# Kernel tuning notes

Measured on AMD Instinct MI355X. Metric: run time of the kernel, lower is better.

Reference implementation:

```python
import jax, jax.numpy as jnp
import numpy as np
from jax import lax

N, C_IN, DIMS, NW, T, H, W = 8, 64, 64, 8, 16, 64, 64
BN_EPS = 1e-5


def setup_inputs() -> dict:
    key = jax.random.key(0)
    ks = jax.random.split(key, 10)
    # kaiming-ish scales
    w_scale = (2.0 / (C_IN * 27)) ** 0.5
    return {
        "x": jax.random.normal(ks[0], (N, C_IN, T, H, W), dtype=jnp.float32),
        "weights": jax.random.normal(ks[1], (NW, DIMS, C_IN, 3, 3, 3), dtype=jnp.float32) * w_scale,
        "biases": jax.random.normal(ks[2], (NW, DIMS), dtype=jnp.float32),
        "se_w1": jax.random.normal(ks[3], (16, C_IN, 5, 5), dtype=jnp.float32) * (2.0 / (C_IN * 25)) ** 0.5,
        "se_b1": jnp.zeros((16,), dtype=jnp.float32),
        "se_w2": jax.random.normal(ks[4], (32, 16, 5, 5), dtype=jnp.float32) * (2.0 / (16 * 25)) ** 0.5,
        "se_b2": jnp.zeros((32,), dtype=jnp.float32),
        "lin_w": jax.random.normal(ks[5], (NW, 32), dtype=jnp.float32) * (1.0 / 32) ** 0.5,
        "lin_b": jnp.zeros((NW,), dtype=jnp.float32),
        "bn_gamma": jnp.ones((DIMS,), dtype=jnp.float32),
        "bn_beta": jnp.zeros((DIMS,), dtype=jnp.float32),
        "epochs_num": 15,
    }


def _forward(x, weights, biases, se_w1, se_b1, se_w2, se_b2, lin_w, lin_b, bn_gamma, bn_beta, epochs_num):
    tau = 30.0 - 2.9 * epochs_num if epochs_num < 10 else 1.0
    # std over temporal axis (torch.std -> unbiased, ddof=1): [n, c, h, w]
    std_x = jnp.std(x, axis=2, ddof=1)
    # squeeze-expand attention branch
    dn2d = ("NCHW", "OIHW", "NCHW")
    h1 = lax.conv_general_dilated(std_x, se_w1, (1, 1), "VALID", dimension_numbers=dn2d)
    h1 = jax.nn.relu(h1 + se_b1[None, :, None, None])
    h2 = lax.conv_general_dilated(h1, se_w2, (1, 1), "VALID", dimension_numbers=dn2d)
    h2 = jax.nn.relu(h2 + se_b2[None, :, None, None])
    pooled = jnp.max(h2, axis=(2, 3))                      # [n, 32]
    logits = pooled @ lin_w.T + lin_b                       # [n, num_weights]
    phi = jax.nn.softmax(logits / tau, axis=1)
    # per-sample dynamic kernels / biases
    dyn_w = jnp.einsum("bn,ncidhw->bcidhw", phi, weights)   # [n, dims, c_in, 3,3,3]
    dyn_b = phi @ biases                                    # [n, dims]
    # grouped conv3d (groups = n) == per-sample conv3d via vmap
    dn3d = ("NCDHW", "OIDHW", "NCDHW")
    def one_conv(xi, wi):
        return lax.conv_general_dilated(xi[None], wi, (1, 1, 1), "SAME", dimension_numbers=dn3d)[0]
    y = jax.vmap(one_conv)(x, dyn_w)                        # [n, dims, t, h, w]
    y = y + dyn_b[:, :, None, None, None]
    # BatchNorm3d (training mode, batch stats, biased var)
    mean = jnp.mean(y, axis=(0, 2, 3, 4))
    var = jnp.var(y, axis=(0, 2, 3, 4))
    b = lambda v: v[None, :, None, None, None]
    y = (y - b(mean)) * b(bn_gamma) * lax.rsqrt(b(var) + BN_EPS) + b(bn_beta)
    return jax.nn.relu(y)


def reference(x, weights, biases, se_w1, se_b1, se_w2, se_b2, lin_w, lin_b, bn_gamma, bn_beta, epochs_num):
    return _forward(x, weights, biases, se_w1, se_b1, se_w2, se_b2, lin_w, lin_b, bn_gamma, bn_beta, epochs_num)
```

## Files before the change

### kernel.cpp

```cpp
#include <hip/hip_runtime.h>
#include <hip/hip_bf16.h>
#include <math.h>

#define N_   8
#define CIN_ 64
#define DIMS_ 64
#define NW_  8
#define T_   16
#define H_   64
#define W_   64
#define HW_  (H_ * W_)
#define THW_ (T_ * HW_)

typedef short bf16x8 __attribute__((ext_vector_type(8)));
typedef float f32x16 __attribute__((ext_vector_type(16)));
typedef int   i32x4v __attribute__((ext_vector_type(4)));
typedef float f32x4v __attribute__((ext_vector_type(4)));

__device__ __forceinline__ unsigned short f2bf(float f) {
    union { float f; unsigned u; } a; a.f = f;
    unsigned r = a.u + 0x7fffu + ((a.u >> 16) & 1u);
    return (unsigned short)(r >> 16);
}
__device__ __forceinline__ float bf2f(unsigned short u) {
    union { unsigned u; float f; } a; a.u = ((unsigned)u) << 16; return a.f;
}

#define CS8_ 8
#define HS8_ (66 * CS8_)
#define TS8_ (10 * HS8_)
#define XSH_ (3 * TS8_)
#define WLH_ (28 * 64 * 8)

__host__ __device__ constexpr int OXc(int tap) {
    int tt = tap > 26 ? 26 : tap;
    return (tt / 9) * TS8_ + ((tt % 9) / 3) * HS8_ + ((tt % 3) - 1) * CS8_;
}

__global__ __launch_bounds__(128) void stdxb_f4(
    const float* __restrict__ x, float* __restrict__ std_x,
    unsigned short* __restrict__ xb, float* __restrict__ sums,
    unsigned* __restrict__ pooled,
    const float* __restrict__ w1, const float* __restrict__ w2,
    float* __restrict__ w1t, float* __restrict__ w2t)
{
    __shared__ unsigned short xsl[16 * 64 * 8];
    const int h = blockIdx.x, c8 = blockIdx.y, n = blockIdx.z;
    const int tid = threadIdx.x;
    const int bf = blockIdx.x + (blockIdx.y << 6) + ((int)blockIdx.z << 9);
    if (bf == 0) {
        sums[tid] = 0.f;
        pooled[tid] = 0u;
        pooled[tid + 128] = 0u;
    }
    if (bf < 300) {
        int i = bf * 128 + tid;
        if (i < 25600) {
            int k = i / 1600, c = (i / 25) % 64, tap = i % 25;
            w1t[(c * 25 + tap) * 16 + k] = w1[i];
        } else if (i < 38400) {
            int j = i - 25600;
            int o = j / 400, c = (j / 25) % 16, tap = j % 25;
            w2t[(c * 25 + tap) * 32 + o] = w2[j];
        }
    }
    const int c = tid >> 4, w4 = tid & 15;
    const int cin = c8 * 8 + c;
    const float* px = x + (((size_t)(n * 64 + cin)) << 16) + (h << 6) + (w4 << 2);
    float s[4] = {0.f, 0.f, 0.f, 0.f}, s2[4] = {0.f, 0.f, 0.f, 0.f};
#pragma unroll
    for (int t = 0; t < T_; ++t) {
        float4 v = *(const float4*)(px + t * HW_);
        float vv[4] = {v.x, v.y, v.z, v.w};
#pragma unroll
        for (int j = 0; j < 4; ++j) {
            s[j] += vv[j];
            s2[j] += vv[j] * vv[j];
            xsl[(t << 9) + (((j << 4) | w4) << 3) + c] = f2bf(vv[j]);
        }
    }
    float4 sd;
#pragma unroll
    for (int j = 0; j < 4; ++j) {
        float var = (s2[j] - s[j] * s[j] * (1.0f / 16.0f)) * (1.0f / 15.0f);
        (&sd.x)[j] = sqrtf(fmaxf(var, 0.f));
    }
    *(float4*)(std_x + (((size_t)(n * 64 + cin)) << 12) + (h << 6) + (w4 << 2)) = sd;
    __syncthreads();
    const int4* src = (const int4*)xsl;
    int4* dst = (int4*)(xb + ((size_t)((n * 8 + c8) * 16) << 12) * 8);
#pragma unroll
    for (int k = 0; k < 8; ++k) {
        int j2 = tid + (k << 7);
        int t = j2 >> 6, q = j2 & 63;
        int ww = ((q & 15) << 2) | (q >> 4);
        dst[((t << 6) + h) * 64 + ww] = src[j2];
    }
}

__global__ __launch_bounds__(256) void se_conv1c(const float* __restrict__ std_x,
        const float* __restrict__ w1t, const float* __restrict__ b1, float* __restrict__ h1) {
    __shared__ float red[3][64][8];
    const int n = blockIdx.y, ks = blockIdx.z * 8;
    const int iq = threadIdx.x & 63, cq = threadIdx.x >> 6;
    const int ij = blockIdx.x * 64 + iq;
    float acc[8];
#pragma unroll
    for (int q = 0; q < 8; ++q) acc[q] = 0.f;
    if (ij < 3600) {
        int i = ij / 60, j = ij - i * 60;
        const float* xn = std_x + (size_t)n * CIN_ * HW_ + i * W_ + j;
        for (int c = cq * 16; c < cq * 16 + 16; ++c) {
            const float* xc = xn + c * HW_;
            float xv[25];
#pragma unroll
            for (int u = 0; u < 5; ++u)
#pragma unroll
                for (int v = 0; v < 5; ++v) xv[u * 5 + v] = xc[u * W_ + v];
            const float* wc = w1t + c * 400 + ks;
#pragma unroll
            for (int tap = 0; tap < 25; ++tap)
#pragma unroll
                for (int q = 0; q < 8; ++q)
                    acc[q] = fmaf(xv[tap], wc[tap * 16 + q], acc[q]);
        }
    }
    if (cq > 0) {
#pragma unroll
        for (int q = 0; q < 8; ++q) red[cq - 1][iq][q] = acc[q];
    }
    __syncthreads();
    if (cq == 0 && ij < 3600) {
#pragma unroll
        for (int q = 0; q < 8; ++q) {
            float a = acc[q] + red[0][iq][q] + red[1][iq][q] + red[2][iq][q] + b1[ks + q];
            h1[((size_t)(n * 16 + ks + q)) * 3600 + ij] = fmaxf(a, 0.f);
        }
    }
}

__global__ __launch_bounds__(256) void se_conv2c(const float* __restrict__ h1,
        const float* __restrict__ w2t, const float* __restrict__ b2,
        unsigned* __restrict__ pooled) {
    __shared__ float red[3][64][8];
    const int n = blockIdx.y, os = blockIdx.z * 8;
    const int iq = threadIdx.x & 63, cq = threadIdx.x >> 6;
    const int ij = blockIdx.x * 64 + iq;
    const int i = ij / 56, j = ij - i * 56;
    float acc[8];
#pragma unroll
    for (int q = 0; q < 8; ++q) acc[q] = 0.f;
    const float* xn = h1 + (size_t)n * 16 * 3600 + i * 60 + j;
    for (int c = cq * 4; c < cq * 4 + 4; ++c) {
        const float* xc = xn + c * 3600;
        float xv[25];
#pragma unroll
        for (int u = 0; u < 5; ++u)
#pragma unroll
            for (int v = 0; v < 5; ++v) xv[u * 5 + v] = xc[u * 60 + v];
        const float* wc = w2t + c * 800 + os;
#pragma unroll
        for (int tap = 0; tap < 25; ++tap)
#pragma unroll
            for (int q = 0; q < 8; ++q)
                acc[q] = fmaf(xv[tap], wc[tap * 32 + q], acc[q]);
    }
    if (cq > 0) {
#pragma unroll
        for (int q = 0; q < 8; ++q) red[cq - 1][iq][q] = acc[q];
    }
    __syncthreads();
    if (cq == 0) {
#pragma unroll
        for (int q = 0; q < 8; ++q) {
            float a = fmaxf(acc[q] + red[0][iq][q] + red[1][iq][q] + red[2][iq][q] + b2[os + q], 0.f);
#pragma unroll
            for (int m = 1; m < 64; m <<= 1) a = fmaxf(a, __shfl_xor(a, m, 64));
            if (iq == 0) atomicMax(&pooled[n * 32 + os + q], __float_as_uint(a));
        }
    }
}

__global__ __launch_bounds__(256) void dyn_w_head(
    const float* __restrict__ weights, const float* __restrict__ pooled,
    const float* __restrict__ lin_w, const float* __restrict__ lin_b,
    const float* __restrict__ biases, const int* __restrict__ epochs,
    unsigned short* __restrict__ wtb2, float* __restrict__ dyn_b) {
    __shared__ float slog[8][8];
    __shared__ float sphi[64];
    const int tid = threadIdx.x;
    const int e = epochs[0];
    const float tau = (e < 10) ? (30.0f - 2.9f * (float)e) : 1.0f;
    if (tid < 64) {
        int b = tid >> 3, m = tid & 7;
        float acc = lin_b[m];
#pragma unroll
        for (int k = 0; k < 32; ++k) acc += pooled[b * 32 + k] * lin_w[m * 32 + k];
        slog[b][m] = acc / tau;
    }
    __syncthreads();
    if (tid < 8) {
        float mx = slog[tid][0];
#pragma unroll
        for (int m = 1; m < 8; ++m) mx = fmaxf(mx, slog[tid][m]);
        float ex[8], ssum = 0.f;
#pragma unroll
        for (int m = 0; m < 8; ++m) { ex[m] = expf(slog[tid][m] - mx); ssum += ex[m]; }
        float inv = 1.0f / ssum;
#pragma unroll
        for (int m = 0; m < 8; ++m) sphi[tid * 8 + m] = ex[m] * inv;
    }
    __syncthreads();
    if (blockIdx.x < 64) {
        int b = blockIdx.x >> 3, c8 = blockIdx.x & 7;
        unsigned* dst = (unsigned*)(wtb2 + (size_t)b * 114688 + (size_t)(c8 * 28 + 27) * 512);
        dst[tid] = 0u;
    }
    if (blockIdx.x == 0) {
#pragma unroll
        for (int idx = tid; idx < 512; idx += 256) {
            int b = idx >> 6, d = idx & 63;
            float a = 0.f;
#pragma unroll
            for (int m = 0; m < 8; ++m) a += sphi[b * 8 + m] * biases[m * DIMS_ + d];
            dyn_b[idx] = a;
        }
    }
    int f = blockIdx.x * 256 + tid;
    if (f >= 110592) return;
    int tap = f % 27, cin = (f / 27) & 63, co = f / 1728;
    float wv[8];
#pragma unroll
    for (int m = 0; m < 8; ++m) wv[m] = weights[(size_t)m * 110592 + f];
    size_t dbase = (size_t)(cin >> 3) * 14336 + tap * 512 + co * 8 + (cin & 7);
#pragma unroll
    for (int b = 0; b < 8; ++b) {
        float acc = 0.f;
#pragma unroll
        for (int m = 0; m < 8; ++m) acc += sphi[b * 8 + m] * wv[m];
        wtb2[(size_t)b * 114688 + dbase] = f2bf(acc);
    }
}

__global__ __launch_bounds__(256, 2) void conv3d_mfma5(
    const unsigned short* __restrict__ xb,
    const unsigned short* __restrict__ wtb2,
    const float* __restrict__ dynb,
    float* __restrict__ y,
    unsigned short* __restrict__ ybf,
    float* __restrict__ sums)
{
    __shared__ __align__(16) unsigned short xs[XSH_];
    __shared__ __align__(16) unsigned short wl[WLH_];
    __shared__ float bnred[128];

    const int flat = blockIdx.x;
    const int n = flat & 7;
    const int hb = (flat >> 3) & 7;
    const int t = flat >> 6;
    const int stag = (((flat >> 3) ^ (flat >> 8)) & 1) * 4;
    const int tid = threadIdx.x;
    const int lane = tid & 63, wid = tid >> 6;
    const int lane31 = lane & 31, tau = lane >> 5;
    const int hbase = hb * 8;

    for (int i = tid; i < XSH_ / 8; i += 256)
        *(int4*)&xs[i * 8] = (int4){0, 0, 0, 0};
    if (tid < 128) bnred[tid] = 0.f;

    const unsigned short* xnb = xb + (size_t)n * 4194304;
    const unsigned short* wnb = wtb2 + (size_t)n * 114688;

    f32x16 acc[2][4];
#pragma unroll
    for (int ci = 0; ci < 2; ++ci)
#pragma unroll
        for (int s = 0; s < 4; ++s)
            acc[ci][s] = (f32x16)(0.f);

    const int aBase = tau * 512 + lane31 * 8;
    int bsp[4];
#pragma unroll
    for (int s = 0; s < 4; ++s)
        bsp[s] = (2 * wid + (s >> 1)) * HS8_ + (1 + (s & 1) * 32 + lane31) * CS8_;

    for (int cc = 0; cc < 8; ++cc) {
        const int c8 = (cc + stag) & 7;
        __syncthreads();
#pragma unroll
        for (int k = 0; k < 7; ++k) {
            int tp = wid + (k << 2);
            const unsigned short* gp = wnb + ((size_t)c8 * 14336 + tp * 512 + lane * 8);
            const unsigned short* lp = &wl[tp * 512];
            __builtin_amdgcn_global_load_lds(
                (const __attribute__((address_space(1))) void*)gp,
                (__attribute__((address_space(3))) void*)lp, 16, 0, 0);
        }
#pragma unroll
        for (int k = 0; k < 8; ++k) {
            int r = wid + (k << 2);
            if (r < 30) {
                int tp = (r >= 20) ? 2 : (r >= 10 ? 1 : 0);
                int hp = r - tp * 10;
                int gt = t + tp - 1, gh = hbase + hp - 1;
                if (((unsigned)gt < 16u) && ((unsigned)gh < 64u)) {
                    const unsigned short* gp = xnb + (size_t)(((c8 * 16 + gt) * 64 + gh) * 64 + lane) * 8;
                    const unsigned short* lp = &xs[tp * TS8_ + hp * HS8_ + CS8_];
                    __builtin_amdgcn_global_load_lds(
                        (const __attribute__((address_space(1))) void*)gp,
                        (__attribute__((address_space(3))) void*)lp, 16, 0, 0);
                }
            }
        }
        __syncthreads();

        __builtin_amdgcn_s_setprio(1);
#pragma unroll
        for (int p = 0; p < 14; ++p) {
            const int xo = tau ? OXc(2 * p + 1) : OXc(2 * p);
            bf16x8 a0 = *(const bf16x8*)&wl[p * 1024 + aBase];
            bf16x8 a1 = *(const bf16x8*)&wl[p * 1024 + aBase + 256];
            bf16x8 b0 = *(const bf16x8*)&xs[bsp[0] + xo];
            bf16x8 b1 = *(const bf16x8*)&xs[bsp[1] + xo];
            bf16x8 b2 = *(const bf16x8*)&xs[bsp[2] + xo];
            bf16x8 b3 = *(const bf16x8*)&xs[bsp[3] + xo];
            acc[0][0] = __builtin_amdgcn_mfma_f32_32x32x16_bf16(a0, b0, acc[0][0], 0, 0, 0);
            acc[0][1] = __builtin_amdgcn_mfma_f32_32x32x16_bf16(a0, b1, acc[0][1], 0, 0, 0);
            acc[0][2] = __builtin_amdgcn_mfma_f32_32x32x16_bf16(a0, b2, acc[0][2], 0, 0, 0);
            acc[0][3] = __builtin_amdgcn_mfma_f32_32x32x16_bf16(a0, b3, acc[0][3], 0, 0, 0);
            acc[1][0] = __builtin_amdgcn_mfma_f32_32x32x16_bf16(a1, b0, acc[1][0], 0, 0, 0);
            acc[1][1] = __builtin_amdgcn_mfma_f32_32x32x16_bf16(a1, b1, acc[1][1], 0, 0, 0);
            acc[1][2] = __builtin_amdgcn_mfma_f32_32x32x16_bf16(a1, b2, acc[1][2], 0, 0, 0);
            acc[1][3] = __builtin_amdgcn_mfma_f32_32x32x16_bf16(a1, b3, acc[1][3], 0, 0, 0);
        }
        __builtin_amdgcn_s_setprio(0);
    }

    const float* db = dynb + n * DIMS_;
    const bool bf = (ybf != nullptr);
#pragma unroll
    for (int ci = 0; ci < 2; ++ci) {
#pragma unroll
        for (int r = 0; r < 16; ++r) {
            const int co = 32 * ci + (r & 3) + 8 * (r >> 2) + 4 * tau;
            const float bco = db[co];
            float ps = 0.f, ps2 = 0.f;
#pragma unroll
            for (int s = 0; s < 4; ++s) {
                float z = acc[ci][s][r] + bco;
                size_t yi = ((size_t)(n * 64 + co) << 16) + ((size_t)t << 12)
                          + ((size_t)(hbase + 2 * wid + (s >> 1)) << 6) + (s & 1) * 32 + lane31;
                if (bf) ybf[yi] = f2bf(z);
                else    y[yi] = z;
                ps += z;
                ps2 += z * z;
            }
#pragma unroll
            for (int m = 1; m < 32; m <<= 1) {
                ps += __shfl_xor(ps, m, 64);
                ps2 += __shfl_xor(ps2, m, 64);
            }
            if (lane31 == 0) {
                atomicAdd(&bnred[co], ps);
                atomicAdd(&bnred[64 + co], ps2);
            }
        }
    }
    __syncthreads();
    if (tid < 128) atomicAdd(&sums[tid], bnred[tid]);
}

__global__ void bn_norm_bf(const float* __restrict__ sums, const float* __restrict__ gamma,
                           const float* __restrict__ beta,
                           const unsigned short* __restrict__ ybf, float* __restrict__ out) {
    const float cnt = (float)(N_ * THW_);
    for (size_t i8 = (size_t)blockIdx.x * 256 + threadIdx.x; i8 < 4194304;
         i8 += (size_t)4096 * 256) {
        int c = (int)((i8 >> 13) & 63);
        float mean = sums[c] / cnt;
        float var = sums[64 + c] / cnt - mean * mean;
        float sc = gamma[c] * rsqrtf(var + 1e-5f);
        float sh = beta[c] - mean * sc;
        i32x4v raw = __builtin_nontemporal_load((const i32x4v*)ybf + i8);
        const unsigned short* u = (const unsigned short*)&raw;
        f32x4v o0, o1;
        o0.x = fmaxf(fmaf(bf2f(u[0]), sc, sh), 0.f);
        o0.y = fmaxf(fmaf(bf2f(u[1]), sc, sh), 0.f);
        o0.z = fmaxf(fmaf(bf2f(u[2]), sc, sh), 0.f);
        o0.w = fmaxf(fmaf(bf2f(u[3]), sc, sh), 0.f);
        o1.x = fmaxf(fmaf(bf2f(u[4]), sc, sh), 0.f);
        o1.y = fmaxf(fmaf(bf2f(u[5]), sc, sh), 0.f);
        o1.z = fmaxf(fmaf(bf2f(u[6]), sc, sh), 0.f);
        o1.w = fmaxf(fmaf(bf2f(u[7]), sc, sh), 0.f);
        __builtin_nontemporal_store(o0, (f32x4v*)out + i8 * 2);
        __builtin_nontemporal_store(o1, (f32x4v*)out + i8 * 2 + 1);
    }
}

__global__ void bn_norm4(const float* __restrict__ sums, const float* __restrict__ gamma,
                         const float* __restrict__ beta, float* __restrict__ y) {
    const float cnt = (float)(N_ * THW_);
    for (size_t idx = (size_t)blockIdx.x * 256 + threadIdx.x; idx < 8388608;
         idx += (size_t)4096 * 256) {
        int c = (int)((idx >> 14) & 63);
        float mean = sums[c] / cnt;
        float var = sums[64 + c] / cnt - mean * mean;
        float sc = gamma[c] * rsqrtf(var + 1e-5f);
        float sh = beta[c] - mean * sc;
        float4 v = ((float4*)y)[idx];
        v.x = fmaxf(fmaf(v.x, sc, sh), 0.f);
        v.y = fmaxf(fmaf(v.y, sc, sh), 0.f);
        v.z = fmaxf(fmaf(v.z, sc, sh), 0.f);
        v.w = fmaxf(fmaf(v.w, sc, sh), 0.f);
        ((float4*)y)[idx] = v;
    }
}

extern "C" void kernel_launch(void* const* d_in, const int* in_sizes, int n_in,
                              void* d_out, int out_size, void* d_ws, size_t ws_size,
                              hipStream_t stream) {
    const float* x       = (const float*)d_in[0];
    const float* weights = (const float*)d_in[1];
    const float* biases  = (const float*)d_in[2];
    const float* se_w1   = (const float*)d_in[3];
    const float* se_b1   = (const float*)d_in[4];
    const float* se_w2   = (const float*)d_in[5];
    const float* se_b2   = (const float*)d_in[6];
    const float* lin_w   = (const float*)d_in[7];
    const float* lin_b   = (const float*)d_in[8];
    const float* gamma   = (const float*)d_in[9];
    const float* beta    = (const float*)d_in[10];
    const int*   epochs  = (const int*)d_in[11];

    float* out = (float*)d_out;
    float* ws = (float*)d_ws;

    const size_t STD_OFF  = 0;
    const size_t H1_OFF   = STD_OFF + 2097152;
    const size_t SUMS_OFF = H1_OFF + 460800;
    const size_t POOL_OFF = SUMS_OFF + 128;
    const size_t PHI_OFF  = POOL_OFF + 256;
    const size_t DYNB_OFF = PHI_OFF + 64;
    const size_t WTB_OFF  = DYNB_OFF + 512;
    const size_t W1T_OFF  = WTB_OFF + 458752;
    const size_t W2T_OFF  = W1T_OFF + 25600;
    const size_t XB_OFF   = W2T_OFF + 12800;
    const size_t YBF_OFF  = XB_OFF + 16777216;
    const size_t NEEDED   = (YBF_OFF + 16777216) * 4;

    float* std_x  = ws + STD_OFF;
    float* h1     = ws + H1_OFF;
    float* sums   = ws + SUMS_OFF;
    float* pooled = ws + POOL_OFF;
    float* dynb   = ws + DYNB_OFF;
    unsigned short* wtb2 = (unsigned short*)(ws + WTB_OFF);
    float* w1t    = ws + W1T_OFF;
    float* w2t    = ws + W2T_OFF;
    unsigned short* xb = (unsigned short*)(ws + XB_OFF);
    unsigned short* ybf = (unsigned short*)(ws + YBF_OFF);

    const bool bf_path = (ws_size >= NEEDED);

    stdxb_f4<<<dim3(64, 8, 8), 128, 0, stream>>>(
        x, std_x, xb, sums, (unsigned*)pooled, se_w1, se_w2, w1t, w2t);

    se_conv1c<<<dim3(57, 8, 2), 256, 0, stream>>>(std_x, w1t, se_b1, h1);
    se_conv2c<<<dim3(49, 8, 4), 256, 0, stream>>>(h1, w2t, se_b2, (unsigned*)pooled);

    dyn_w_head<<<432, 256, 0, stream>>>(weights, pooled, lin_w, lin_b, biases, epochs,
                                        wtb2, dynb);

    conv3d_mfma5<<<1024, 256, 0, stream>>>(
        xb, wtb2, dynb, out, bf_path ? ybf : nullptr, sums);

    if (bf_path)
        bn_norm_bf<<<4096, 256, 0, stream>>>(sums, gamma, beta, ybf, out);
    else
        bn_norm4<<<4096, 256, 0, stream>>>(sums, gamma, beta, out);
}
```

Before: 371.8 us.

## Fuse conv3d and BN normalize into one persistent kernel with grid-wide spin barrier

Replaces the separate conv3d and BN-normalize launches with a single 512-block kernel. Each block computes two time slices, accumulates BN statistics, and increments a global counter. The last block computes scale and shift and releases the others through a spin flag, after which each block normalizes its own bf16 outputs into the fp32 result. This removes one kernel launch and lets blocks reread their freshly written intermediate while it may still be cached. In exchange it relies on all 512 blocks being co-resident (checked through the occupancy query), halves the grid, and makes every block wait idle at the barrier.

```diff
diff --git a/kernel.cpp b/kernel.cpp
--- a/kernel.cpp
+++ b/kernel.cpp
@@ -40,7 +40,7 @@
 __global__ __launch_bounds__(128) void stdxb_f4(
     const float* __restrict__ x, float* __restrict__ std_x,
     unsigned short* __restrict__ xb, float* __restrict__ sums,
-    unsigned* __restrict__ pooled,
+    unsigned* __restrict__ pooled, unsigned* __restrict__ ctrflag,
     const float* __restrict__ w1, const float* __restrict__ w2,
     float* __restrict__ w1t, float* __restrict__ w2t)
 {
@@ -52,6 +52,7 @@
         sums[tid] = 0.f;
         pooled[tid] = 0u;
         pooled[tid + 128] = 0u;
+        if (tid < 2) ctrflag[tid] = 0u;
     }
     if (bf < 300) {
         int i = bf * 128 + tid;
@@ -242,13 +243,204 @@
     }
 }
 
-__global__ __launch_bounds__(256, 2) void conv3d_mfma5(
+__global__ __launch_bounds__(256, 2) void conv3d_spin(
     const unsigned short* __restrict__ xb,
     const unsigned short* __restrict__ wtb2,
     const float* __restrict__ dynb,
-    float* __restrict__ y,
     unsigned short* __restrict__ ybf,
-    float* __restrict__ sums)
+    float* __restrict__ out,
+    float* __restrict__ sums,
+    float* __restrict__ gscsh,
+    unsigned* __restrict__ ctrflag,
+    const float* __restrict__ gamma,
+    const float* __restrict__ beta)
+{
+    __shared__ __align__(16) unsigned short xs[XSH_];
+    __shared__ __align__(16) unsigned short wl[WLH_];
+    __shared__ float bnred[128];
+    __shared__ float scshL[128];
+    __shared__ unsigned isLast;
+
+    const int flat = blockIdx.x;
+    const int n = flat & 7;
+    const int hb = (flat >> 3) & 7;
+    const int t0 = (flat >> 6) * 2;
+    const int stag = (((flat >> 3) ^ (flat >> 8)) & 1) * 4;
+    const int tid = threadIdx.x;
+    const int lane = tid & 63, wid = tid >> 6;
+    const int lane31 = lane & 31, tau = lane >> 5;
+    const int hbase = hb * 8;
+
+    for (int i = tid; i < XSH_ / 8; i += 256)
+        *(int4*)&xs[i * 8] = (int4){0, 0, 0, 0};
+    if (tid < 128) bnred[tid] = 0.f;
+
+    const unsigned short* xnb = xb + (size_t)n * 4194304;
+    const unsigned short* wnb = wtb2 + (size_t)n * 114688;
+
+    const int aBase = tau * 512 + lane31 * 8;
+    int bsp[4];
+#pragma unroll
+    for (int s = 0; s < 4; ++s)
+        bsp[s] = (2 * wid + (s >> 1)) * HS8_ + (1 + (s & 1) * 32 + lane31) * CS8_;
+
+    const float* db = dynb + n * DIMS_;
+
+    for (int tt = 0; tt < 2; ++tt) {
+        const int t = t0 + tt;
+        if (tt == 1 && t == 15) {
+            __syncthreads();
+            for (int i = tid; i < TS8_ / 8; i += 256)
+                *(int4*)&xs[2 * TS8_ + i * 8] = (int4){0, 0, 0, 0};
+        }
+
+        f32x16 acc[2][4];
+#pragma unroll
+        for (int ci = 0; ci < 2; ++ci)
+#pragma unroll
+            for (int s = 0; s < 4; ++s)
+                acc[ci][s] = (f32x16)(0.f);
+
+        for (int cc = 0; cc < 8; ++cc) {
+            const int c8 = (cc + stag) & 7;
+            __syncthreads();
+#pragma unroll
+            for (int k = 0; k < 7; ++k) {
+                int tp = wid + (k << 2);
+                const unsigned short* gp = wnb + ((size_t)c8 * 14336 + tp * 512 + lane * 8);
+                const unsigned short* lp = &wl[tp * 512];
+                __builtin_amdgcn_global_load_lds(
+                    (const __attribute__((address_space(1))) void*)gp,
+                    (__attribute__((address_space(3))) void*)lp, 16, 0, 0);
+            }
+#pragma unroll
+            for (int k = 0; k < 8; ++k) {
+                int r = wid + (k << 2);
+                if (r < 30) {
+                    int tp = (r >= 20) ? 2 : (r >= 10 ? 1 : 0);
+                    int hp = r - tp * 10;
+                    int gt = t + tp - 1, gh = hbase + hp - 1;
+                    if (((unsigned)gt < 16u) && ((unsigned)gh < 64u)) {
+                        const unsigned short* gp = xnb + (size_t)(((c8 * 16 + gt) * 64 + gh) * 64 + lane) * 8;
+                        const unsigned short* lp = &xs[tp * TS8_ + hp * HS8_ + CS8_];
+                        __builtin_amdgcn_global_load_lds(
+                            (const __attribute__((address_space(1))) void*)gp,
+                            (__attribute__((address_space(3))) void*)lp, 16, 0, 0);
+                    }
+                }
+            }
+            __syncthreads();
+
+            __builtin_amdgcn_s_setprio(1);
+#pragma unroll
+            for (int p = 0; p < 14; ++p) {
+                const int xo = tau ? OXc(2 * p + 1) : OXc(2 * p);
+                bf16x8 a0 = *(const bf16x8*)&wl[p * 1024 + aBase];
+                bf16x8 a1 = *(const bf16x8*)&wl[p * 1024 + aBase + 256];
+                bf16x8 b0 = *(const bf16x8*)&xs[bsp[0] + xo];
+                bf16x8 b1 = *(const bf16x8*)&xs[bsp[1] + xo];
+                bf16x8 b2 = *(const bf16x8*)&xs[bsp[2] + xo];
+                bf16x8 b3 = *(const bf16x8*)&xs[bsp[3] + xo];
+                acc[0][0] = __builtin_amdgcn_mfma_f32_32x32x16_bf16(a0, b0, acc[0][0], 0, 0, 0);
+                acc[0][1] = __builtin_amdgcn_mfma_f32_32x32x16_bf16(a0, b1, acc[0][1], 0, 0, 0);
+                acc[0][2] = __builtin_amdgcn_mfma_f32_32x32x16_bf16(a0, b2, acc[0][2], 0, 0, 0);
+                acc[0][3] = __builtin_amdgcn_mfma_f32_32x32x16_bf16(a0, b3, acc[0][3], 0, 0, 0);
+                acc[1][0] = __builtin_amdgcn_mfma_f32_32x32x16_bf16(a1, b0, acc[1][0], 0, 0, 0);
+                acc[1][1] = __builtin_amdgcn_mfma_f32_32x32x16_bf16(a1, b1, acc[1][1], 0, 0, 0);
+                acc[1][2] = __builtin_amdgcn_mfma_f32_32x32x16_bf16(a1, b2, acc[1][2], 0, 0, 0);
+                acc[1][3] = __builtin_amdgcn_mfma_f32_32x32x16_bf16(a1, b3, acc[1][3], 0, 0, 0);
+            }
+            __builtin_amdgcn_s_setprio(0);
+        }
+
+#pragma unroll
+        for (int ci = 0; ci < 2; ++ci) {
+#pragma unroll
+            for (int r = 0; r < 16; ++r) {
+                const int co = 32 * ci + (r & 3) + 8 * (r >> 2) + 4 * tau;
+                const float bco = db[co];
+                float ps = 0.f, ps2 = 0.f;
+#pragma unroll
+                for (int s = 0; s < 4; ++s) {
+                    float z = acc[ci][s][r] + bco;
+                    size_t yi = ((size_t)(n * 64 + co) << 16) + ((size_t)t << 12)
+                              + ((size_t)(hbase + 2 * wid + (s >> 1)) << 6) + (s & 1) * 32 + lane31;
+                    ybf[yi] = f2bf(z);
+                    ps += z;
+                    ps2 += z * z;
+                }
+#pragma unroll
+                for (int m = 1; m < 32; m <<= 1) {
+                    ps += __shfl_xor(ps, m, 64);
+                    ps2 += __shfl_xor(ps2, m, 64);
+                }
+                if (lane31 == 0) {
+                    atomicAdd(&bnred[co], ps);
+                    atomicAdd(&bnred[64 + co], ps2);
+                }
+            }
+        }
+    }
+
+    __syncthreads();
+    if (tid < 128) atomicAdd(&sums[tid], bnred[tid]);
+    __threadfence();
+    __syncthreads();
+    if (tid == 0) isLast = (atomicAdd(&ctrflag[0], 1u) == 511u) ? 1u : 0u;
+    __syncthreads();
+    if (isLast) {
+        if (tid < 64) {
+            const float cnt = (float)(N_ * THW_);
+            float s = atomicAdd(&sums[tid], 0.f);
+            float s2 = atomicAdd(&sums[64 + tid], 0.f);
+            float mean = s / cnt;
+            float var = s2 / cnt - mean * mean;
+            float sc = gamma[tid] * rsqrtf(var + 1e-5f);
+            gscsh[tid] = sc;
+            gscsh[64 + tid] = beta[tid] - mean * sc;
+        }
+        __threadfence();
+        __syncthreads();
+        if (tid == 0) atomicExch(&ctrflag[1], 1u);
+    }
+    if (tid == 0) {
+        while (atomicAdd(&ctrflag[1], 0u) == 0u) __builtin_amdgcn_s_sleep(32);
+    }
+    __syncthreads();
+    if (tid < 128) scshL[tid] = atomicAdd(&gscsh[tid], 0.f);
+    __syncthreads();
+
+    for (int tt = 0; tt < 2; ++tt) {
+        const int t = t0 + tt;
+        const size_t tbase = ((size_t)(n * 64) << 16) + ((size_t)t << 12) + ((size_t)hbase << 6);
+#pragma unroll
+        for (int it = 0; it < 16; ++it) {
+            int g = it * 256 + tid;
+            int co = g >> 6;
+            int rem = g & 63;
+            size_t addr = tbase + ((size_t)co << 16) + (size_t)rem * 8;
+            i32x4v raw = __builtin_nontemporal_load((const i32x4v*)(ybf + addr));
+            const unsigned short* u = (const unsigned short*)&raw;
+            float sc = scshL[co], sh = scshL[64 + co];
+            f32x4v o0, o1;
+            o0.x = fmaxf(fmaf(bf2f(u[0]), sc, sh), 0.f);
+            o0.y = fmaxf(fmaf(bf2f(u[1]), sc, sh), 0.f);
+            o0.z = fmaxf(fmaf(bf2f(u[2]), sc, sh), 0.f);
+            o0.w = fmaxf(fmaf(bf2f(u[3]), sc, sh), 0.f);
+            o1.x = fmaxf(fmaf(bf2f(u[4]), sc, sh), 0.f);
+            o1.y = fmaxf(fmaf(bf2f(u[5]), sc, sh), 0.f);
+            o1.z = fmaxf(fmaf(bf2f(u[6]), sc, sh), 0.f);
+            o1.w = fmaxf(fmaf(bf2f(u[7]), sc, sh), 0.f);
+            __builtin_nontemporal_store(o0, (f32x4v*)(out + addr));
+            __builtin_nontemporal_store(o1, (f32x4v*)(out + addr + 4));
+        }
+    }
+}
+
+__global__ __launch_bounds__(256, 2) void conv3d_mfma5(
+    const unsigned short* __restrict__ xb, const unsigned short* __restrict__ wtb2,
+    const float* __restrict__ dynb, float* __restrict__ y,
+    unsigned short* __restrict__ ybf, float* __restrict__ sums)
 {
     __shared__ __align__(16) unsigned short xs[XSH_];
     __shared__ __align__(16) unsigned short wl[WLH_];
@@ -452,6 +644,7 @@
     float* h1     = ws + H1_OFF;
     float* sums   = ws + SUMS_OFF;
     float* pooled = ws + POOL_OFF;
+    unsigned* ctrflag = (unsigned*)(ws + PHI_OFF);
     float* dynb   = ws + DYNB_OFF;
     unsigned short* wtb2 = (unsigned short*)(ws + WTB_OFF);
     float* w1t    = ws + W1T_OFF;
@@ -461,8 +654,12 @@
 
     const bool bf_path = (ws_size >= NEEDED);
 
+    int occ = 0;
+    hipOccupancyMaxActiveBlocksPerMultiprocessor(&occ, conv3d_spin, 256, 0);
+    const bool spin_ok = bf_path && (occ >= 2);
+
     stdxb_f4<<<dim3(64, 8, 8), 128, 0, stream>>>(
-        x, std_x, xb, sums, (unsigned*)pooled, se_w1, se_w2, w1t, w2t);
+        x, std_x, xb, sums, (unsigned*)pooled, ctrflag, se_w1, se_w2, w1t, w2t);
 
     se_conv1c<<<dim3(57, 8, 2), 256, 0, stream>>>(std_x, w1t, se_b1, h1);
     se_conv2c<<<dim3(49, 8, 4), 256, 0, stream>>>(h1, w2t, se_b2, (unsigned*)pooled);
@@ -470,11 +667,14 @@
     dyn_w_head<<<432, 256, 0, stream>>>(weights, pooled, lin_w, lin_b, biases, epochs,
                                         wtb2, dynb);
 
-    conv3d_mfma5<<<1024, 256, 0, stream>>>(
-        xb, wtb2, dynb, out, bf_path ? ybf : nullptr, sums);
-
-    if (bf_path)
+    if (spin_ok) {
+        conv3d_spin<<<512, 256, 0, stream>>>(xb, wtb2, dynb, ybf, out, sums,
+                                             pooled, ctrflag, gamma, beta);
+    } else if (bf_path) {
+        conv3d_mfma5<<<1024, 256, 0, stream>>>(xb, wtb2, dynb, out, ybf, sums);
         bn_norm_bf<<<4096, 256, 0, stream>>>(sums, gamma, beta, ybf, out);
-    else
+    } else {
+        conv3d_mfma5<<<1024, 256, 0, stream>>>(xb, wtb2, dynb, out, nullptr, sums);
         bn_norm4<<<4096, 256, 0, stream>>>(sums, gamma, beta, out);
-}
+    }
+}
```

Result: no change. 371.7 us (-0.0%).

## Recompute conv3d in a second pass instead of storing intermediate y

Applied to the files above, without the earlier changes.

Splits the conv into a stats-only pass that accumulates per-channel sums, a tiny finalize kernel that computes scale/shift, and a second conv pass that recomputes the convolution and writes normalized ReLU output directly. This removes the write and re-read of the full intermediate activation tensor (bf16 or fp32) at the cost of doing the MFMA convolution twice. It pays off only if the conv is cheap relative to that memory traffic. The pooled buffer is reused to hold scale/shift after the SE branch has consumed it.

```diff
diff --git a/kernel.cpp b/kernel.cpp
--- a/kernel.cpp
+++ b/kernel.cpp
@@ -14,16 +14,11 @@
 
 typedef short bf16x8 __attribute__((ext_vector_type(8)));
 typedef float f32x16 __attribute__((ext_vector_type(16)));
-typedef int   i32x4v __attribute__((ext_vector_type(4)));
-typedef float f32x4v __attribute__((ext_vector_type(4)));
 
 __device__ __forceinline__ unsigned short f2bf(float f) {
     union { float f; unsigned u; } a; a.f = f;
     unsigned r = a.u + 0x7fffu + ((a.u >> 16) & 1u);
     return (unsigned short)(r >> 16);
-}
-__device__ __forceinline__ float bf2f(unsigned short u) {
-    union { unsigned u; float f; } a; a.u = ((unsigned)u) << 16; return a.f;
 }
 
 #define CS8_ 8
@@ -242,12 +237,10 @@
     }
 }
 
-__global__ __launch_bounds__(256, 2) void conv3d_mfma5(
+__global__ __launch_bounds__(256, 2) void conv3d_stats(
     const unsigned short* __restrict__ xb,
     const unsigned short* __restrict__ wtb2,
     const float* __restrict__ dynb,
-    float* __restrict__ y,
-    unsigned short* __restrict__ ybf,
     float* __restrict__ sums)
 {
     __shared__ __align__(16) unsigned short xs[XSH_];
@@ -337,7 +330,6 @@
     }
 
     const float* db = dynb + n * DIMS_;
-    const bool bf = (ybf != nullptr);
 #pragma unroll
     for (int ci = 0; ci < 2; ++ci) {
 #pragma unroll
@@ -348,10 +340,6 @@
 #pragma unroll
             for (int s = 0; s < 4; ++s) {
                 float z = acc[ci][s][r] + bco;
-                size_t yi = ((size_t)(n * 64 + co) << 16) + ((size_t)t << 12)
-                          + ((size_t)(hbase + 2 * wid + (s >> 1)) << 6) + (s & 1) * 32 + lane31;
-                if (bf) ybf[yi] = f2bf(z);
-                else    y[yi] = z;
                 ps += z;
                 ps2 += z * z;
             }
@@ -370,49 +358,124 @@
     if (tid < 128) atomicAdd(&sums[tid], bnred[tid]);
 }
 
-__global__ void bn_norm_bf(const float* __restrict__ sums, const float* __restrict__ gamma,
-                           const float* __restrict__ beta,
-                           const unsigned short* __restrict__ ybf, float* __restrict__ out) {
+__global__ void bn_fin(const float* __restrict__ sums, const float* __restrict__ gamma,
+                       const float* __restrict__ beta, float* __restrict__ scsh) {
+    int c = threadIdx.x;
     const float cnt = (float)(N_ * THW_);
-    for (size_t i8 = (size_t)blockIdx.x * 256 + threadIdx.x; i8 < 4194304;
-         i8 += (size_t)4096 * 256) {
-        int c = (int)((i8 >> 13) & 63);
-        float mean = sums[c] / cnt;
-        float var = sums[64 + c] / cnt - mean * mean;
-        float sc = gamma[c] * rsqrtf(var + 1e-5f);
-        float sh = beta[c] - mean * sc;
-        i32x4v raw = __builtin_nontemporal_load((const i32x4v*)ybf + i8);
-        const unsigned short* u = (const unsigned short*)&raw;
-        f32x4v o0, o1;
-        o0.x = fmaxf(fmaf(bf2f(u[0]), sc, sh), 0.f);
-        o0.y = fmaxf(fmaf(bf2f(u[1]), sc, sh), 0.f);
-        o0.z = fmaxf(fmaf(bf2f(u[2]), sc, sh), 0.f);
-        o0.w = fmaxf(fmaf(bf2f(u[3]), sc, sh), 0.f);
-        o1.x = fmaxf(fmaf(bf2f(u[4]), sc, sh), 0.f);
-        o1.y = fmaxf(fmaf(bf2f(u[5]), sc, sh), 0.f);
-        o1.z = fmaxf(fmaf(bf2f(u[6]), sc, sh), 0.f);
-        o1.w = fmaxf(fmaf(bf2f(u[7]), sc, sh), 0.f);
-        __builtin_nontemporal_store(o0, (f32x4v*)out + i8 * 2);
-        __builtin_nontemporal_store(o1, (f32x4v*)out + i8 * 2 + 1);
-    }
-}
-
-__global__ void bn_norm4(const float* __restrict__ sums, const float* __restrict__ gamma,
-                         const float* __restrict__ beta, float* __restrict__ y) {
-    const float cnt = (float)(N_ * THW_);
-    for (size_t idx = (size_t)blockIdx.x * 256 + threadIdx.x; idx < 8388608;
-         idx += (size_t)4096 * 256) {
-        int c = (int)((idx >> 14) & 63);
-        float mean = sums[c] / cnt;
-        float var = sums[64 + c] / cnt - mean * mean;
-        float sc = gamma[c] * rsqrtf(var + 1e-5f);
-        float sh = beta[c] - mean * sc;
-        float4 v = ((float4*)y)[idx];
-        v.x = fmaxf(fmaf(v.x, sc, sh), 0.f);
-        v.y = fmaxf(fmaf(v.y, sc, sh), 0.f);
-        v.z = fmaxf(fmaf(v.z, sc, sh), 0.f);
-        v.w = fmaxf(fmaf(v.w, sc, sh), 0.f);
-        ((float4*)y)[idx] = v;
+    float mean = sums[c] / cnt;
+    float var = sums[64 + c] / cnt - mean * mean;
+    float sc = gamma[c] * rsqrtf(var + 1e-5f);
+    scsh[c] = sc;
+    scsh[64 + c] = beta[c] - mean * sc;
+}
+
+__global__ __launch_bounds__(256, 2) void conv3d_norm(
+    const unsigned short* __restrict__ xb,
+    const unsigned short* __restrict__ wtb2,
+    const float* __restrict__ dynb,
+    const float* __restrict__ scsh,
+    float* __restrict__ out)
+{
+    __shared__ __align__(16) unsigned short xs[XSH_];
+    __shared__ __align__(16) unsigned short wl[WLH_];
+
+    const int flat = blockIdx.x;
+    const int n = flat & 7;
+    const int hb = (flat >> 3) & 7;
+    const int t = flat >> 6;
+    const int stag = (((flat >> 3) ^ (flat >> 8)) & 1) * 4;
+    const int tid = threadIdx.x;
+    const int lane = tid & 63, wid = tid >> 6;
+    const int lane31 = lane & 31, tau = lane >> 5;
+    const int hbase = hb * 8;
+
+    for (int i = tid; i < XSH_ / 8; i += 256)
+        *(int4*)&xs[i * 8] = (int4){0, 0, 0, 0};
+
+    const unsigned short* xnb = xb + (size_t)n * 4194304;
+    const unsigned short* wnb = wtb2 + (size_t)n * 114688;
+
+    f32x16 acc[2][4];
+#pragma unroll
+    for (int ci = 0; ci < 2; ++ci)
+#pragma unroll
+        for (int s = 0; s < 4; ++s)
+            acc[ci][s] = (f32x16)(0.f);
+
+    const int aBase = tau * 512 + lane31 * 8;
+    int bsp[4];
+#pragma unroll
+    for (int s = 0; s < 4; ++s)
+        bsp[s] = (2 * wid + (s >> 1)) * HS8_ + (1 + (s & 1) * 32 + lane31) * CS8_;
+
+    for (int cc = 0; cc < 8; ++cc) {
+        const int c8 = (cc + stag) & 7;
+        __syncthreads();
+#pragma unroll
+        for (int k = 0; k < 7; ++k) {
+            int tp = wid + (k << 2);
+            const unsigned short* gp = wnb + ((size_t)c8 * 14336 + tp * 512 + lane * 8);
+            const unsigned short* lp = &wl[tp * 512];
+            __builtin_amdgcn_global_load_lds(
+                (const __attribute__((address_space(1))) void*)gp,
+                (__attribute__((address_space(3))) void*)lp, 16, 0, 0);
+        }
+#pragma unroll
+        for (int k = 0; k < 8; ++k) {
+            int r = wid + (k << 2);
+            if (r < 30) {
+                int tp = (r >= 20) ? 2 : (r >= 10 ? 1 : 0);
+                int hp = r - tp * 10;
+                int gt = t + tp - 1, gh = hbase + hp - 1;
+                if (((unsigned)gt < 16u) && ((unsigned)gh < 64u)) {
+                    const unsigned short* gp = xnb + (size_t)(((c8 * 16 + gt) * 64 + gh) * 64 + lane) * 8;
+                    const unsigned short* lp = &xs[tp * TS8_ + hp * HS8_ + CS8_];
+                    __builtin_amdgcn_global_load_lds(
+                        (const __attribute__((address_space(1))) void*)gp,
+                        (__attribute__((address_space(3))) void*)lp, 16, 0, 0);
+                }
+            }
+        }
+        __syncthreads();
+
+        __builtin_amdgcn_s_setprio(1);
+#pragma unroll
+        for (int p = 0; p < 14; ++p) {
+            const int xo = tau ? OXc(2 * p + 1) : OXc(2 * p);
+            bf16x8 a0 = *(const bf16x8*)&wl[p * 1024 + aBase];
+            bf16x8 a1 = *(const bf16x8*)&wl[p * 1024 + aBase + 256];
+            bf16x8 b0 = *(const bf16x8*)&xs[bsp[0] + xo];
+            bf16x8 b1 = *(const bf16x8*)&xs[bsp[1] + xo];
+            bf16x8 b2 = *(const bf16x8*)&xs[bsp[2] + xo];
+            bf16x8 b3 = *(const bf16x8*)&xs[bsp[3] + xo];
+            acc[0][0] = __builtin_amdgcn_mfma_f32_32x32x16_bf16(a0, b0, acc[0][0], 0, 0, 0);
+            acc[0][1] = __builtin_amdgcn_mfma_f32_32x32x16_bf16(a0, b1, acc[0][1], 0, 0, 0);
+            acc[0][2] = __builtin_amdgcn_mfma_f32_32x32x16_bf16(a0, b2, acc[0][2], 0, 0, 0);
+            acc[0][3] = __builtin_amdgcn_mfma_f32_32x32x16_bf16(a0, b3, acc[0][3], 0, 0, 0);
+            acc[1][0] = __builtin_amdgcn_mfma_f32_32x32x16_bf16(a1, b0, acc[1][0], 0, 0, 0);
+            acc[1][1] = __builtin_amdgcn_mfma_f32_32x32x16_bf16(a1, b1, acc[1][1], 0, 0, 0);
+            acc[1][2] = __builtin_amdgcn_mfma_f32_32x32x16_bf16(a1, b2, acc[1][2], 0, 0, 0);
+            acc[1][3] = __builtin_amdgcn_mfma_f32_32x32x16_bf16(a1, b3, acc[1][3], 0, 0, 0);
+        }
+        __builtin_amdgcn_s_setprio(0);
+    }
+
+    const float* db = dynb + n * DIMS_;
+#pragma unroll
+    for (int ci = 0; ci < 2; ++ci) {
+#pragma unroll
+        for (int r = 0; r < 16; ++r) {
+            const int co = 32 * ci + (r & 3) + 8 * (r >> 2) + 4 * tau;
+            const float sc = scsh[co];
+            const float sh = fmaf(db[co], sc, scsh[64 + co]);
+#pragma unroll
+            for (int s = 0; s < 4; ++s) {
+                float v = fmaxf(fmaf(acc[ci][s][r], sc, sh), 0.f);
+                size_t yi = ((size_t)(n * 64 + co) << 16) + ((size_t)t << 12)
+                          + ((size_t)(hbase + 2 * wid + (s >> 1)) << 6) + (s & 1) * 32 + lane31;
+                out[yi] = v;
+            }
+        }
     }
 }
 
@@ -439,14 +502,11 @@
     const size_t H1_OFF   = STD_OFF + 2097152;
     const size_t SUMS_OFF = H1_OFF + 460800;
     const size_t POOL_OFF = SUMS_OFF + 128;
-    const size_t PHI_OFF  = POOL_OFF + 256;
-    const size_t DYNB_OFF = PHI_OFF + 64;
+    const size_t DYNB_OFF = POOL_OFF + 256;
     const size_t WTB_OFF  = DYNB_OFF + 512;
     const size_t W1T_OFF  = WTB_OFF + 458752;
     const size_t W2T_OFF  = W1T_OFF + 25600;
     const size_t XB_OFF   = W2T_OFF + 12800;
-    const size_t YBF_OFF  = XB_OFF + 16777216;
-    const size_t NEEDED   = (YBF_OFF + 16777216) * 4;
 
     float* std_x  = ws + STD_OFF;
     float* h1     = ws + H1_OFF;
@@ -457,9 +517,6 @@
     float* w1t    = ws + W1T_OFF;
     float* w2t    = ws + W2T_OFF;
     unsigned short* xb = (unsigned short*)(ws + XB_OFF);
-    unsigned short* ybf = (unsigned short*)(ws + YBF_OFF);
-
-    const bool bf_path = (ws_size >= NEEDED);
 
     stdxb_f4<<<dim3(64, 8, 8), 128, 0, stream>>>(
         x, std_x, xb, sums, (unsigned*)pooled, se_w1, se_w2, w1t, w2t);
@@ -470,11 +527,7 @@
     dyn_w_head<<<432, 256, 0, stream>>>(weights, pooled, lin_w, lin_b, biases, epochs,
                                         wtb2, dynb);
 
-    conv3d_mfma5<<<1024, 256, 0, stream>>>(
-        xb, wtb2, dynb, out, bf_path ? ybf : nullptr, sums);
-
-    if (bf_path)
-        bn_norm_bf<<<4096, 256, 0, stream>>>(sums, gamma, beta, ybf, out);
-    else
-        bn_norm4<<<4096, 256, 0, stream>>>(sums, gamma, beta, out);
-}
+    conv3d_stats<<<1024, 256, 0, stream>>>(xb, wtb2, dynb, sums);
+    bn_fin<<<1, 64, 0, stream>>>(sums, gamma, beta, pooled);
+    conv3d_norm<<<1024, 256, 0, stream>>>(xb, wtb2, dynb, pooled, out);
+}
```

After: 421.6 us. 13.4% more time.
